# Performance work log

Hardware: AMD Instinct MI355X
Metric: run time of the kernel (lower is better)

The kernel has to match this reference:

```python
import jax, jax.numpy as jnp
import numpy as np


def setup_inputs() -> dict:
    key = jax.random.key(0)
    k1, k2, k3 = jax.random.split(key, 3)
    B, C, T = 2048, 32000, 16384
    preds = jax.random.normal(k1, (B, C), dtype=jnp.float32)
    flat_targets = jax.random.randint(k2, (T,), 0, C, dtype=jnp.int64)
    row_ids = jnp.sort(jax.random.randint(k3, (T,), 0, B, dtype=jnp.int64))
    return {"preds": preds, "flat_targets": flat_targets, "row_ids": row_ids}


def reference(preds, flat_targets, row_ids):
    # Original: softmax(preds) then per-sample gather -> log -> sum, then
    # sum over batch / batch_size. softmax+log fused as log_softmax; the
    # ragged per-sample sums collapse into a single global sum since the
    # loss is sum over all gathered targets divided by batch_size.
    logp = jax.nn.log_softmax(preds, axis=1)          # [B, C]
    nll = -logp[row_ids, flat_targets]                # [T] ragged gather
    batch_size = preds.shape[0]
    return nll.sum() / batch_size
```

## Files before the change

### kernel.cpp

```cpp
#include <hip/hip_runtime.h>
#include <hip/hip_bf16.h>
#include <math.h>

constexpr int kC  = 32000;
constexpr int kN4 = kC / 4;
constexpr int kNT = 256;

__device__ __forceinline__ int lower_bound_wave(const int* __restrict__ rows,
                                                int T, int key, int lane,
                                                int L, int len) {
    while (len > 0) {
        int q = L + ((lane * len) >> 6);
        int v = (q < T) ? rows[q] : 0x7fffffff;
        unsigned long long b = __ballot(v < key);
        if (b == 0) break;
        int c = (int)__popcll(b);
        int qlast = L + (((c - 1) * len) >> 6);
        int qff   = (c < 64) ? (L + ((c * len) >> 6)) : (L + len);
        L   = qlast + 1;
        len = qff - qlast;
    }
    return L;
}

__global__ __launch_bounds__(kNT) void row_lse_gather_kernel(
    const float* __restrict__ preds, const int* __restrict__ tgt,
    const int* __restrict__ rows, float* __restrict__ partial,
    int T) {
    const int row  = blockIdx.x;
    const size_t base = (size_t)row * kC;
    const float4* __restrict__ p = reinterpret_cast<const float4*>(preds + base);
    const int lane = threadIdx.x & 63;
    const int wave = threadIdx.x >> 6;

    float s0 = 0.f, s1 = 0.f, s2 = 0.f, s3 = 0.f;
    float4 v = p[threadIdx.x];
    for (int j = threadIdx.x + kNT; j < kN4; j += kNT) {
        float4 nv = p[j];
        s0 += __expf(v.x);
        s1 += __expf(v.y);
        s2 += __expf(v.z);
        s3 += __expf(v.w);
        v = nv;
    }
    s0 += __expf(v.x);
    s1 += __expf(v.y);
    s2 += __expf(v.z);
    s3 += __expf(v.w);

    float s = (s0 + s1) + (s2 + s3);
    #pragma unroll
    for (int off = 32; off > 0; off >>= 1) s += __shfl_xor(s, off);

    __shared__ float ss[4];
    if (lane == 0) ss[wave] = s;
    __syncthreads();

    if (wave == 0) {
        float S = ss[0] + ss[1] + ss[2] + ss[3];
        float lse = __logf(S);

        const int lo  = lower_bound_wave(rows, T, row,     lane, 0,  T);
        const int hi  = lower_bound_wave(rows, T, row + 1, lane, lo, T - lo);
        const int cnt = hi - lo;

        float g = 0.f;
        for (int j = lo + lane; j < hi; j += 64)
            g += preds[base + tgt[j]];
        #pragma unroll
        for (int off = 32; off > 0; off >>= 1) g += __shfl_xor(g, off);

        if (lane == 0) partial[row] = (float)cnt * lse - g;
    }
}

__global__ __launch_bounds__(256) void finalize_kernel(
    const float* __restrict__ partial, float* __restrict__ out,
    int B, float invB) {
    float a = 0.f;
    for (int i = threadIdx.x; i < B; i += 256) a += partial[i];
    #pragma unroll
    for (int off = 32; off > 0; off >>= 1) a += __shfl_xor(a, off);

    __shared__ float ws[4];
    const int wave = threadIdx.x >> 6;
    if ((threadIdx.x & 63) == 0) ws[wave] = a;
    __syncthreads();
    if (threadIdx.x == 0)
        out[0] = (ws[0] + ws[1] + ws[2] + ws[3]) * invB;
}

extern "C" void kernel_launch(void* const* d_in, const int* in_sizes, int n_in,
                              void* d_out, int out_size, void* d_ws, size_t ws_size,
                              hipStream_t stream) {
    const float* preds = (const float*)d_in[0];
    const int*   tgt   = (const int*)d_in[1];
    const int*   rows  = (const int*)d_in[2];
    float* out = (float*)d_out;

    const int T = in_sizes[1];
    const int B = in_sizes[0] / kC;

    float* partial = (float*)d_ws;

    row_lse_gather_kernel<<<B, kNT, 0, stream>>>(preds, tgt, rows, partial, T);
    finalize_kernel<<<1, 256, 0, stream>>>(partial, out, B, 1.0f / (float)B);
}
```

Baseline: 48.35 us.

## Overlap target search/gather with exp-sum and fuse finalize via atomicAdd

Wave 0 now performs the row-range binary search and target gather before its reduced share of the exp-sum, while the other three waves take larger contiguous chunks of the row. This hides the serial search/gather latency behind the streaming reduction instead of running it after the barrier. The separate finalize kernel is removed; each block atomically adds its scaled contribution to the output after a memset. This makes the float summation order nondeterministic.

```diff
diff --git a/kernel.cpp b/kernel.cpp
--- a/kernel.cpp
+++ b/kernel.cpp
@@ -5,6 +5,11 @@
 constexpr int kC  = 32000;
 constexpr int kN4 = kC / 4;
 constexpr int kNT = 256;
+
+constexpr int kIt0    = 26;
+constexpr int kItN    = 33;
+constexpr int kStart1 = kIt0 * 64;
+constexpr int kChunk  = kItN * 64;
 
 __device__ __forceinline__ int lower_bound_wave(const int* __restrict__ rows,
                                                 int T, int key, int lane,
@@ -23,20 +28,34 @@
     return L;
 }
 
-__global__ __launch_bounds__(kNT) void row_lse_gather_kernel(
+__global__ __launch_bounds__(kNT) void ce_loss_kernel(
     const float* __restrict__ preds, const int* __restrict__ tgt,
-    const int* __restrict__ rows, float* __restrict__ partial,
-    int T) {
+    const int* __restrict__ rows, float* __restrict__ out,
+    int T, float invB) {
     const int row  = blockIdx.x;
     const size_t base = (size_t)row * kC;
     const float4* __restrict__ p = reinterpret_cast<const float4*>(preds + base);
     const int lane = threadIdx.x & 63;
     const int wave = threadIdx.x >> 6;
 
+    float g = 0.f;
+    int cnt = 0;
+    if (wave == 0) {
+        const int lo = lower_bound_wave(rows, T, row,     lane, 0,  T);
+        const int hi = lower_bound_wave(rows, T, row + 1, lane, lo, T - lo);
+        cnt = hi - lo;
+        for (int j = lo + lane; j < hi; j += 64)
+            g += preds[base + tgt[j]];
+    }
+
+    const int nIt   = (wave == 0) ? kIt0 : kItN;
+    const int start = (wave == 0) ? 0 : kStart1 + (wave - 1) * kChunk;
+
     float s0 = 0.f, s1 = 0.f, s2 = 0.f, s3 = 0.f;
-    float4 v = p[threadIdx.x];
-    for (int j = threadIdx.x + kNT; j < kN4; j += kNT) {
-        float4 nv = p[j];
+    int idx = start + lane;
+    float4 v = p[idx];
+    for (int k = 1; k < nIt; ++k) {
+        float4 nv = p[idx + k * 64];
         s0 += __expf(v.x);
         s1 += __expf(v.y);
         s2 += __expf(v.z);
@@ -57,37 +76,15 @@
     __syncthreads();
 
     if (wave == 0) {
-        float S = ss[0] + ss[1] + ss[2] + ss[3];
-        float lse = __logf(S);
-
-        const int lo  = lower_bound_wave(rows, T, row,     lane, 0,  T);
-        const int hi  = lower_bound_wave(rows, T, row + 1, lane, lo, T - lo);
-        const int cnt = hi - lo;
-
-        float g = 0.f;
-        for (int j = lo + lane; j < hi; j += 64)
-            g += preds[base + tgt[j]];
         #pragma unroll
         for (int off = 32; off > 0; off >>= 1) g += __shfl_xor(g, off);
-
-        if (lane == 0) partial[row] = (float)cnt * lse - g;
+        if (lane == 0) {
+            float S   = ss[0] + ss[1] + ss[2] + ss[3];
+            float lse = __logf(S);
+            float val = (float)cnt * lse - g;
+            atomicAdd(out, val * invB);
+        }
     }
-}
-
-__global__ __launch_bounds__(256) void finalize_kernel(
-    const float* __restrict__ partial, float* __restrict__ out,
-    int B, float invB) {
-    float a = 0.f;
-    for (int i = threadIdx.x; i < B; i += 256) a += partial[i];
-    #pragma unroll
-    for (int off = 32; off > 0; off >>= 1) a += __shfl_xor(a, off);
-
-    __shared__ float ws[4];
-    const int wave = threadIdx.x >> 6;
-    if ((threadIdx.x & 63) == 0) ws[wave] = a;
-    __syncthreads();
-    if (threadIdx.x == 0)
-        out[0] = (ws[0] + ws[1] + ws[2] + ws[3]) * invB;
 }
 
 extern "C" void kernel_launch(void* const* d_in, const int* in_sizes, int n_in,
@@ -101,8 +98,8 @@
     const int T = in_sizes[1];
     const int B = in_sizes[0] / kC;
 
-    float* partial = (float*)d_ws;
+    hipMemsetAsync(out, 0, sizeof(float), stream);
 
-    row_lse_gather_kernel<<<B, kNT, 0, stream>>>(preds, tgt, rows, partial, T);
-    finalize_kernel<<<1, 256, 0, stream>>>(partial, out, B, 1.0f / (float)B);
+    ce_loss_kernel<<<B, kNT, 0, stream>>>(preds, tgt, rows, out,
+                                          T, 1.0f / (float)B);
 }
```

Result: slower. 68.15 us (+41.0%).
